# Kernel optimization log

Hardware: AMD Instinct MI355X
Metric: run time of the kernel (lower is better)

Reference implementation:

```python
import jax, jax.numpy as jnp
import numpy as np

NUM_HEADS = 8
EPS = 1e-5  # torch GroupNorm default eps


def setup_inputs() -> dict:
    key = jax.random.key(0)
    ks = jax.random.split(key, 3)
    B, C, H, W = 8, 384, 32, 32
    x = jax.random.normal(ks[0], (B, C, H, W), dtype=jnp.float32)
    qkv_w = jax.random.normal(ks[1], (3 * C, C), dtype=jnp.float32) * 0.02
    proj_w = jax.random.normal(ks[2], (C, C), dtype=jnp.float32) * 0.02
    proj_b = jnp.zeros((C,), dtype=jnp.float32)
    lambda_param = jnp.ones((1, NUM_HEADS, 1, 1), dtype=jnp.float32) * 0.5
    gc = NUM_HEADS * ((C // NUM_HEADS) // 2)  # 192 group-norm channels
    gn_weight = jnp.ones((gc,), dtype=jnp.float32)
    gn_bias = jnp.zeros((gc,), dtype=jnp.float32)
    return {"x": x, "qkv_w": qkv_w, "lambda_param": lambda_param,
            "gn_weight": gn_weight, "gn_bias": gn_bias,
            "proj_w": proj_w, "proj_b": proj_b}


def reference(x, qkv_w, lambda_param, gn_weight, gn_bias, proj_w, proj_b):
    B, C, H, W = x.shape
    nh = NUM_HEADS
    hd = C // nh
    hd2 = hd // 2
    N = H * W
    scale = hd ** -0.5

    xf = x.reshape(B, C, N)
    qkv = jnp.einsum('oc,bcn->bon', qkv_w, xf)  # (B, 3C, N), 1x1 conv no bias
    q, k, v = jnp.split(qkv, 3, axis=1)
    q = q.reshape(B, nh, hd, N)
    k = k.reshape(B, nh, hd, N)
    v = v.reshape(B, nh, hd, N)

    q1, q2 = q[:, :, :hd2], q[:, :, hd2:]
    k1, k2 = k[:, :, :hd2], k[:, :, hd2:]
    v1, v2 = v[:, :, :hd2], v[:, :, hd2:]

    # GroupNorm(2 groups) on q2 viewed as (B, nh*hd2, H, W)
    gc = nh * hd2
    qg = q2.reshape(B, 2, (gc // 2) * N)  # normalize over (group channels, H, W)
    mean = qg.mean(axis=2, keepdims=True)
    var = qg.var(axis=2, keepdims=True)
    qg = (qg - mean) * jax.lax.rsqrt(var + EPS)
    q2n = qg.reshape(B, gc, N) * gn_weight[None, :, None] + gn_bias[None, :, None]
    q2n = q2n.reshape(B, nh, hd2, N)

    # dual softmax attention maps (B, nh, N, N)
    attn1 = jax.nn.softmax(jnp.einsum('bhdn,bhdm->bhnm', q1, k1) * scale, axis=-1)
    attn2 = jax.nn.softmax(jnp.einsum('bhdn,bhdm->bhnm', q2n, k2) * scale * lambda_param, axis=-1)
    diff = attn1 - attn2

    out1 = jnp.einsum('bhnm,bhdm->bhnd', diff, v1)  # (B, nh, N, hd2)
    out2 = jnp.einsum('bhnm,bhdm->bhnd', diff, v2)
    out = jnp.concatenate([out1, out2], axis=2)  # (B, nh, 2N, hd2) -- matches torch cat dim=2
    out = out.reshape(B, C, H, W)

    out = jnp.einsum('oc,bchw->bohw', proj_w, out) + proj_b[None, :, None, None]
    return out
```

## Files before the change

### kernel.cpp

```cpp
#include <hip/hip_runtime.h>
#include <hip/hip_bf16.h>
#include <stdint.h>

typedef _Float16 half8 __attribute__((ext_vector_type(8)));
typedef _Float16 half4 __attribute__((ext_vector_type(4)));
typedef __fp16 fp16x2 __attribute__((ext_vector_type(2)));
typedef float floatx4 __attribute__((ext_vector_type(4)));
typedef float floatx16 __attribute__((ext_vector_type(16)));

#define SCALE 0.14433756729740643f
#define LOG2E 1.4426950408889634f


__device__ inline float fexp2(float x) { return __builtin_exp2f(x); }

__device__ inline uint32_t pkrtz(float a, float b) {
  fp16x2 h = __builtin_amdgcn_cvt_pkrtz(a, b);
  union { fp16x2 h; uint32_t u; } cv; cv.h = h; return cv.u;
}

__launch_bounds__(256)
__global__ void k_prep(const float* __restrict__ qkv_w, const float* __restrict__ pw,
                       const float* __restrict__ x, _Float16* __restrict__ Wf,
                       _Float16* __restrict__ PWf, _Float16* __restrict__ Xt) {
  const int bid = blockIdx.x;
  if (bid < 288) {
    const float* src = (bid < 216) ? qkv_w : pw;
    _Float16* dst = (bid < 216) ? Wf : PWf;
    int cid = (bid < 216 ? bid : bid - 216) * 256 + threadIdx.x;
    int nchunks = (bid < 216) ? 55296 : 18432;
    if (cid >= nchunks) return;
    int lane = cid & 63;
    int t = cid >> 6;
    int cb = t % 12;
    int g16 = t / 12;
    const float* s = src + (long)(g16 * 16 + (lane & 15)) * 384 + cb * 32 + (lane >> 4) * 8;
    floatx4 a = *(const floatx4*)s;
    floatx4 b = *(const floatx4*)(s + 4);
    half8 h;
    #pragma unroll
    for (int j = 0; j < 4; j++) { h[j] = (_Float16)a[j]; h[j+4] = (_Float16)b[j]; }
    *(half8*)(dst + (long)cid * 8) = h;
  } else {
    int idx = bid - 288;
    const int cblk = idx % 12, nseg = (idx / 12) & 3, b = idx / 48;
    const float* S = x + ((long)b * 384 + cblk * 32) * 1024 + nseg * 256;
    _Float16* D = Xt + (long)b * 393216 + cblk * 32768 + (long)nseg * 256 * 32;
    __shared__ _Float16 T[32][264];
    const int wv = threadIdx.x >> 6, lane = threadIdx.x & 63;
    #pragma unroll
    for (int rr = 0; rr < 8; rr++) {
      int r = wv * 8 + rr;
      floatx4 v = *(const floatx4*)(S + (long)r * 1024 + lane * 4);
      half4 h;
      #pragma unroll
      for (int j = 0; j < 4; j++) h[j] = (_Float16)v[j];
      *(half4*)&T[r][lane * 4] = h;
    }
    __syncthreads();
    const int nn = threadIdx.x >> 3, c = (threadIdx.x & 7) * 4;
    #pragma unroll
    for (int p = 0; p < 8; p++) {
      int n = p * 32 + nn;
      half4 h;
      #pragma unroll
      for (int i = 0; i < 4; i++) h[i] = T[c + i][n];
      *(half4*)(D + (long)n * 32 + c) = h;
    }
  }
}

__launch_bounds__(256)
__global__ void k_tr(const float* __restrict__ src, _Float16* __restrict__ dst) {
  const int cblk = blockIdx.x, nseg = blockIdx.y, b = blockIdx.z;
  const float* S = src + ((long)b * 384 + cblk * 32) * 1024 + nseg * 256;
  _Float16* D = dst + (long)b * 393216 + cblk * 32768 + (long)nseg * 256 * 32;
  __shared__ _Float16 T[32][264];
  const int wv = threadIdx.x >> 6, lane = threadIdx.x & 63;
  #pragma unroll
  for (int rr = 0; rr < 8; rr++) {
    int r = wv * 8 + rr;
    floatx4 v = *(const floatx4*)(S + (long)r * 1024 + lane * 4);
    half4 h;
    #pragma unroll
    for (int j = 0; j < 4; j++) h[j] = (_Float16)v[j];
    *(half4*)&T[r][lane * 4] = h;
  }
  __syncthreads();
  const int nn = threadIdx.x >> 3, c = (threadIdx.x & 7) * 4;
  #pragma unroll
  for (int p = 0; p < 8; p++) {
    int n = p * 32 + nn;
    half4 h;
    #pragma unroll
    for (int i = 0; i < 4; i++) h[i] = T[c + i][n];
    *(half4*)(D + (long)n * 32 + c) = h;
  }
}

__launch_bounds__(256, 4)
__global__ void k_qkv(const _Float16* __restrict__ Xt, const _Float16* __restrict__ Wf,
                      _Float16* __restrict__ Qs, _Float16* __restrict__ Ks,
                      _Float16* __restrict__ Vs) {
  const int tid = threadIdx.x;
  const int lane = tid & 63;
  const int wv = tid >> 6;
  const int l15 = lane & 15;
  const int g = lane >> 4;
  const int o0 = blockIdx.x * 48;
  const int n0 = blockIdx.y * 64;
  const int b = blockIdx.z;

  const int ncol = n0 + wv * 16 + l15;
  const _Float16* xp = Xt + (long)b * 393216 + (long)ncol * 32 + g * 8;
  const _Float16* wfb = Wf + (long)(blockIdx.x * 36) * 512 + lane * 8;

  half8 xb[12];
  #pragma unroll
  for (int cb = 0; cb < 12; cb++) xb[cb] = *(const half8*)(xp + cb * 32768);

  floatx4 zero4 = {0.f, 0.f, 0.f, 0.f};
  floatx4 acc0 = zero4, acc1 = zero4, acc2 = zero4;

  half8 A0 = *(const half8*)(wfb);
  half8 A1 = *(const half8*)(wfb + 12 * 512);
  half8 A2 = *(const half8*)(wfb + 24 * 512);
  #pragma unroll
  for (int cb = 0; cb < 12; cb++) {
    half8 c0 = A0, c1 = A1, c2 = A2;
    if (cb < 11) {
      A0 = *(const half8*)(wfb + (cb + 1) * 512);
      A1 = *(const half8*)(wfb + (12 + cb + 1) * 512);
      A2 = *(const half8*)(wfb + (24 + cb + 1) * 512);
    }
    acc0 = __builtin_amdgcn_mfma_f32_16x16x32_f16(c0, xb[cb], acc0, 0, 0, 0);
    acc1 = __builtin_amdgcn_mfma_f32_16x16x32_f16(c1, xb[cb], acc1, 0, 0, 0);
    acc2 = __builtin_amdgcn_mfma_f32_16x16x32_f16(c2, xb[cb], acc2, 0, 0, 0);
  }

  floatx4 acc[3] = {acc0, acc1, acc2};
  __shared__ __align__(16) _Float16 T[3456];

  if (o0 < 768) {
    #pragma unroll
    for (int rt = 0; rt < 3; rt++)
      #pragma unroll
      for (int r = 0; r < 4; r++)
        T[(wv * 16 + l15) * 52 + rt * 16 + g * 4 + r] = (_Float16)acc[rt][r];
    __syncthreads();
    const int qk = o0 >= 384;
    const int hh = (o0 - qk * 384) / 48;
    _Float16* base = (qk ? Ks : Qs) + (long)(b * 8 + hh) * 65536;
    #pragma unroll
    for (int it = 0; it < 2; it++) {
      int slot = it * 256 + tid;
      int ntl = slot >> 8;
      int t   = (slot >> 6) & 3;
      int ln  = slot & 63;
      int hi_s = ln >> 5, l31_s = ln & 31;
      int n_ = ntl * 32 + l31_s;
      int c0 = t * 16 + hi_s * 8;
      half8 val;
      #pragma unroll
      for (int j = 0; j < 8; j++) {
        int col = c0 + j;
        int d48 = col < 24 ? col : col - 8;
        bool isq = (col < 24) || (col >= 32 && col < 56);
        val[j] = isq ? T[n_ * 52 + d48] : (_Float16)0;
      }
      *(half8*)(base + ((((n0 >> 5) + ntl) * 4 + t) * 64 + ln) * 8) = val;
    }
  } else {
    #pragma unroll
    for (int rt = 0; rt < 3; rt++)
      #pragma unroll
      for (int r = 0; r < 4; r++)
        T[(rt * 16 + g * 4 + r) * 72 + wv * 16 + l15] = (_Float16)acc[rt][r];
    __syncthreads();
    const int hh = (o0 - 768) / 48;
    _Float16* base = Vs + (long)(b * 8 + hh) * 65536;
    #pragma unroll
    for (int it = 0; it < 2; it++) {
      int slot = it * 256 + tid;
      int lwin = slot >> 8;
      int ckc  = (slot >> 6) & 3;
      int kc   = ckc & 1, c = ckc >> 1;
      int ln = slot & 63;
      int hi_s = ln >> 5, l31_s = ln & 31;
      int d48 = c * 32 + l31_s;
      half8 val;
      if (d48 < 48) {
        int mb = lwin * 32 + kc * 16 + hi_s * 4;
        half4 a = *(const half4*)&T[d48 * 72 + mb];
        half4 bq = *(const half4*)&T[d48 * 72 + mb + 8];
        val[0] = a[0]; val[1] = a[1]; val[2] = a[2]; val[3] = a[3];
        val[4] = bq[0]; val[5] = bq[1]; val[6] = bq[2]; val[7] = bq[3];
      } else {
        _Float16 f = (d48 == 48) ? (_Float16)1 : (_Float16)0;
        #pragma unroll
        for (int j = 0; j < 8; j++) val[j] = f;
      }
      *(half8*)(base + ((((n0 >> 5) + lwin) * 4 + ckc) * 64 + ln) * 8) = val;
    }
  }
}

__global__ void k_gnstats(const _Float16* __restrict__ Qs, float* __restrict__ partial) {
  int bg = blockIdx.x >> 3;
  int chunk = blockIdx.x & 7;
  int b = bg >> 1, grp = bg & 1;
  float s1 = 0.f, s2 = 0.f;
  #pragma unroll
  for (int k = 0; k < 6; k++) {
    int f = chunk * 1536 + k * 256 + threadIdx.x;
    int uid = f / 96;
    int slot = f - uid * 96;
    int h = grp * 4 + (uid >> 5);
    int ntile = uid & 31;
    int t = slot < 64 ? 2 : 3;
    int ln = slot < 64 ? slot : slot - 64;
    const _Float16* p = Qs + (long)(b * 8 + h) * 65536 + ((ntile * 4 + t) * 64 + ln) * 8;
    half8 v = *(const half8*)p;
    #pragma unroll
    for (int j = 0; j < 8; j++) { float x = (float)v[j]; s1 += x; s2 += x * x; }
  }
  #pragma unroll
  for (int off = 32; off > 0; off >>= 1) {
    s1 += __shfl_down(s1, off);
    s2 += __shfl_down(s2, off);
  }
  __shared__ float red[8];
  int wv = threadIdx.x >> 6;
  if ((threadIdx.x & 63) == 0) { red[wv] = s1; red[4 + wv] = s2; }
  __syncthreads();
  if (threadIdx.x == 0) {
    float S1 = red[0] + red[1] + red[2] + red[3];
    float S2 = red[4] + red[5] + red[6] + red[7];
    partial[blockIdx.x * 2]     = S1;
    partial[blockIdx.x * 2 + 1] = S2;
  }
}

__launch_bounds__(512, 4)
__global__ void k_attn(const _Float16* __restrict__ Qs, const _Float16* __restrict__ Ks,
                       const _Float16* __restrict__ Vs, const float* __restrict__ partial,
                       const float* __restrict__ lam, const float* __restrict__ gw,
                       const float* __restrict__ gb, float* __restrict__ Y) {
  const int tid = threadIdx.x;
  const int lane = tid & 63;
  const int wv = tid >> 6;
  const int l31 = lane & 31;
  const int hi = lane >> 5;
  const int id = blockIdx.x;
  const int bh = ((id >> 6) << 3) | (id & 7);
  const int ntlgrp = (id >> 3) & 7;
  const int br = wv & 1;
  const int ntile = ntlgrp * 4 + (wv >> 1);
  const int n0 = ntile * 32;
  const int b = bh >> 3, h = bh & 7;

  const _Float16* Qp = Qs + (long)bh * 65536 + (ntile * 256 + lane) * 8;
  half8 qra = *(const half8*)(Qp + (2 * br) * 512);
  half8 qrb = *(const half8*)(Qp + (2 * br + 1) * 512);
  half8 qfa, qfb;
  if (br == 0) {
    const float s1s = SCALE * LOG2E;
    #pragma unroll
    for (int j = 0; j < 8; j++) {
      qfa[j] = (_Float16)((float)qra[j] * s1s);
      qfb[j] = (_Float16)((float)qrb[j] * s1s);
    }
  } else {
    const int grp = h >> 2;
    const float* pp = partial + (b * 2 + grp) * 16;
    float S1 = 0.f, S2 = 0.f;
    #pragma unroll
    for (int i = 0; i < 8; i++) { S1 += pp[2*i]; S2 += pp[2*i+1]; }
    float mean = S1 * (1.f / 98304.f);
    float rstd = rsqrtf(S2 * (1.f / 98304.f) - mean * mean + 1e-5f);
    float sl = SCALE * LOG2E * lam[h];
    const float* gwp = gw + h * 24;
    const float* gbp = gb + h * 24;
    #pragma unroll
    for (int j = 0; j < 8; j++) {
      qfa[j] = (_Float16)((((float)qra[j] - mean) * rstd * gwp[hi * 8 + j] + gbp[hi * 8 + j]) * sl);
      qfb[j] = (_Float16)((((float)qrb[j] - mean) * rstd * gwp[16 + j] + gbp[16 + j]) * sl);
    }
  }

  const _Float16* gK = Ks + (long)bh * 65536 + ((wv >> 2) * 2048 + (wv & 3) * 512) + lane * 8;
  const _Float16* gV = Vs + (long)bh * 65536 + ((wv >> 2) * 2048 + (wv & 3) * 512) + lane * 8;

  __shared__ __align__(16) char smem[32768];
  const int ldsK = wv * 1024 + lane * 16;
  const int ldsV = 8192 + wv * 1024 + lane * 16;

  floatx16 z16;
  #pragma unroll
  for (int i = 0; i < 16; i++) z16[i] = 0.f;
  floatx16 accA = z16, accB = z16;

  {
    uint4 a = *(const uint4*)gK;
    uint4 c = *(const uint4*)gV;
    *(uint4*)(smem + ldsK) = a;
    *(uint4*)(smem + ldsV) = c;
  }
  __syncthreads();

  #pragma unroll 2
  for (int i = 0; i < 16; i++) {
    const int cur = (i & 1) << 14;
    uint4 sa, sc;
    if (i < 15) {
      sa = *(const uint4*)(gK + (i + 1) * 4096);
      sc = *(const uint4*)(gV + (i + 1) * 4096);
    }
    #pragma unroll
    for (int j = 0; j < 2; j++) {
      const char* Kb = smem + cur + j * 4096;
      const char* Vb = smem + cur + 8192 + j * 4096;
      half8 kfa = *(const half8*)(Kb + (2 * br) * 1024 + lane * 16);
      half8 kfb = *(const half8*)(Kb + (2 * br + 1) * 1024 + lane * 16);

      floatx16 s = __builtin_amdgcn_mfma_f32_32x32x16_f16(kfa, qfa, z16, 0, 0, 0);
      s = __builtin_amdgcn_mfma_f32_32x32x16_f16(kfb, qfb, s, 0, 0, 0);

      half8 vf0 = *(const half8*)(Vb + lane * 16);
      half8 vf1 = *(const half8*)(Vb + 1024 + lane * 16);
      half8 vf2 = *(const half8*)(Vb + 2048 + lane * 16);
      half8 vf3 = *(const half8*)(Vb + 3072 + lane * 16);

      uint32_t u[8];
      #pragma unroll
      for (int q = 0; q < 8; q++)
        u[q] = pkrtz(fexp2(s[2 * q]), fexp2(s[2 * q + 1]));

      union { uint32_t u[4]; half8 h; } pa;
      pa.u[0] = u[0]; pa.u[1] = u[1]; pa.u[2] = u[2]; pa.u[3] = u[3];
      half8 pc0 = pa.h;
      pa.u[0] = u[4]; pa.u[1] = u[5]; pa.u[2] = u[6]; pa.u[3] = u[7];
      half8 pc1 = pa.h;

      accA = __builtin_amdgcn_mfma_f32_32x32x16_f16(pc0, vf0, accA, 0, 0, 0);
      accA = __builtin_amdgcn_mfma_f32_32x32x16_f16(pc1, vf1, accA, 0, 0, 0);
      accB = __builtin_amdgcn_mfma_f32_32x32x16_f16(pc0, vf2, accB, 0, 0, 0);
      accB = __builtin_amdgcn_mfma_f32_32x32x16_f16(pc1, vf3, accB, 0, 0, 0);
    }
    if (i < 15) {
      *(uint4*)(smem + (cur ^ 16384) + ldsK) = sa;
      *(uint4*)(smem + (cur ^ 16384) + ldsV) = sc;
    }
    __syncthreads();
  }

  const int pairid = wv >> 1;
  float* rbuf = (float*)(smem + pairid * 8192);
  if (br == 1) {
    #pragma unroll
    for (int r = 0; r < 16; r++) {
      rbuf[r * 64 + lane] = accA[r];
      rbuf[(16 + r) * 64 + lane] = accB[r];
    }
  }
  __syncthreads();
  if (br == 0) {
    float a2a[16], a2b[16];
    #pragma unroll
    for (int r = 0; r < 16; r++) {
      a2a[r] = rbuf[r * 64 + lane];
      a2b[r] = rbuf[(16 + r) * 64 + lane];
    }
    float* Ybh = Y + (long)bh * 49152;
    const int src = (lane & 32) + 16;
    #pragma unroll
    for (int r = 0; r < 16; r++) {
      float i1 = __builtin_amdgcn_rcpf(__shfl(accB[r], src));
      float i2 = __builtin_amdgcn_rcpf(__shfl(a2b[r], src));
      int n = n0 + (r & 3) + 8 * ((r >> 2) & 3) + 4 * hi;
      float o0 = accA[r] * i1 - a2a[r] * i2;
      float o1 = accB[r] * i1 - a2b[r] * i2;
      int p0 = l31 >= 24;
      Ybh[p0 * 24576 + n * 24 + (l31 - p0 * 24)] = o0;
      if (l31 < 16) Ybh[24576 + n * 24 + 8 + l31] = o1;
    }
  }
}

__launch_bounds__(256, 4)
__global__ void k_proj(const _Float16* __restrict__ Yt, const _Float16* __restrict__ PWf,
                       const float* __restrict__ PB, float* __restrict__ out) {
  const int tid = threadIdx.x, lane = tid & 63, wv = tid >> 6, l15 = lane & 15, g = lane >> 4;
  const int o0 = blockIdx.x * 64, m0 = blockIdx.y * 64, b = blockIdx.z;

  const int mcol = m0 + wv * 16 + l15;
  const _Float16* yp = Yt + (long)b * 393216 + (long)mcol * 32 + g * 8;
  const _Float16* wfb = PWf + (long)(blockIdx.x * 48) * 512 + lane * 8;

  half8 yb[12];
  #pragma unroll
  for (int cb = 0; cb < 12; cb++) yb[cb] = *(const half8*)(yp + cb * 32768);

  floatx4 zero4 = {0.f, 0.f, 0.f, 0.f};
  floatx4 acc0 = zero4, acc1 = zero4, acc2 = zero4, acc3 = zero4;

  half8 A0 = *(const half8*)(wfb);
  half8 A1 = *(const half8*)(wfb + 12 * 512);
  half8 A2 = *(const half8*)(wfb + 24 * 512);
  half8 A3 = *(const half8*)(wfb + 36 * 512);
  #pragma unroll
  for (int cb = 0; cb < 12; cb++) {
    half8 c0 = A0, c1 = A1, c2 = A2, c3 = A3;
    if (cb < 11) {
      A0 = *(const half8*)(wfb + (cb + 1) * 512);
      A1 = *(const half8*)(wfb + (12 + cb + 1) * 512);
      A2 = *(const half8*)(wfb + (24 + cb + 1) * 512);
      A3 = *(const half8*)(wfb + (36 + cb + 1) * 512);
    }
    acc0 = __builtin_amdgcn_mfma_f32_16x16x32_f16(c0, yb[cb], acc0, 0, 0, 0);
    acc1 = __builtin_amdgcn_mfma_f32_16x16x32_f16(c1, yb[cb], acc1, 0, 0, 0);
    acc2 = __builtin_amdgcn_mfma_f32_16x16x32_f16(c2, yb[cb], acc2, 0, 0, 0);
    acc3 = __builtin_amdgcn_mfma_f32_16x16x32_f16(c3, yb[cb], acc3, 0, 0, 0);
  }

  floatx4 acc[4] = {acc0, acc1, acc2, acc3};
  #pragma unroll
  for (int rt = 0; rt < 4; rt++) {
    int o_ = o0 + rt * 16 + g * 4;
    #pragma unroll
    for (int r = 0; r < 4; r++) {
      out[(long)(b * 384 + o_ + r) * 1024 + mcol] = acc[rt][r] + PB[o_ + r];
    }
  }
}

extern "C" void kernel_launch(void* const* d_in, const int* in_sizes, int n_in,
                              void* d_out, int out_size, void* d_ws, size_t ws_size,
                              hipStream_t stream) {
  const float* x     = (const float*)d_in[0];
  const float* qkv_w = (const float*)d_in[1];
  const float* lam   = (const float*)d_in[2];
  const float* gw    = (const float*)d_in[3];
  const float* gb    = (const float*)d_in[4];
  const float* pw    = (const float*)d_in[5];
  const float* pb    = (const float*)d_in[6];
  float* out = (float*)d_out;
  char* ws = (char*)d_ws;
  _Float16* Qs  = (_Float16*)ws;
  _Float16* Ks  = (_Float16*)(ws + 8388608);
  _Float16* Vs  = (_Float16*)(ws + 16777216);
  float* Y        = (float*)(ws + 25165824);
  float* partial  = (float*)(ws + 37748736);
  _Float16* Xt  = (_Float16*)(ws + 37752832);
  _Float16* Yt  = (_Float16*)(ws + 44044288);
  _Float16* Wf  = (_Float16*)(ws + 50335744);
  _Float16* PWf = (_Float16*)(ws + 51220480);

  hipLaunchKernelGGL(k_prep,    dim3(672),        dim3(256), 0, stream, qkv_w, pw, x, Wf, PWf, Xt);
  hipLaunchKernelGGL(k_qkv,     dim3(24, 16, 8),  dim3(256), 0, stream, Xt, Wf, Qs, Ks, Vs);
  hipLaunchKernelGGL(k_gnstats, dim3(128),        dim3(256), 0, stream, Qs, partial);
  hipLaunchKernelGGL(k_attn,    dim3(512),        dim3(512), 0, stream, Qs, Ks, Vs, partial, lam, gw, gb, Y);
  hipLaunchKernelGGL(k_tr,      dim3(12, 4, 8),   dim3(256), 0, stream, Y, Yt);
  hipLaunchKernelGGL(k_proj,    dim3(6, 16, 8),   dim3(256), 0, stream, Yt, PWf, pb, out);
}
```

Before: 96.01 us.

## Fuse GroupNorm stats into QKV kernel and transpose output into attention epilogue

Computes per-block GroupNorm partial sums inside the QKV GEMM from the shared-memory tile, removing the separate stats kernel and its re-read of Q. The attention epilogue now writes fp16 output directly in the transposed layout the projection kernel consumes, removing the fp32 intermediate and the transpose kernel. This drops two launches and a round-trip of the intermediate through global memory. The cost is scattered 2-byte stores from attention and an extra reduction and barrier in the QKV blocks.

Result: slower. 97.94 us (+2.0%).

```diff
diff --git a/kernel.cpp b/kernel.cpp
--- a/kernel.cpp
+++ b/kernel.cpp
@@ -70,38 +70,10 @@
   }
 }
 
-__launch_bounds__(256)
-__global__ void k_tr(const float* __restrict__ src, _Float16* __restrict__ dst) {
-  const int cblk = blockIdx.x, nseg = blockIdx.y, b = blockIdx.z;
-  const float* S = src + ((long)b * 384 + cblk * 32) * 1024 + nseg * 256;
-  _Float16* D = dst + (long)b * 393216 + cblk * 32768 + (long)nseg * 256 * 32;
-  __shared__ _Float16 T[32][264];
-  const int wv = threadIdx.x >> 6, lane = threadIdx.x & 63;
-  #pragma unroll
-  for (int rr = 0; rr < 8; rr++) {
-    int r = wv * 8 + rr;
-    floatx4 v = *(const floatx4*)(S + (long)r * 1024 + lane * 4);
-    half4 h;
-    #pragma unroll
-    for (int j = 0; j < 4; j++) h[j] = (_Float16)v[j];
-    *(half4*)&T[r][lane * 4] = h;
-  }
-  __syncthreads();
-  const int nn = threadIdx.x >> 3, c = (threadIdx.x & 7) * 4;
-  #pragma unroll
-  for (int p = 0; p < 8; p++) {
-    int n = p * 32 + nn;
-    half4 h;
-    #pragma unroll
-    for (int i = 0; i < 4; i++) h[i] = T[c + i][n];
-    *(half4*)(D + (long)n * 32 + c) = h;
-  }
-}
-
 __launch_bounds__(256, 4)
 __global__ void k_qkv(const _Float16* __restrict__ Xt, const _Float16* __restrict__ Wf,
                       _Float16* __restrict__ Qs, _Float16* __restrict__ Ks,
-                      _Float16* __restrict__ Vs) {
+                      _Float16* __restrict__ Vs, float* __restrict__ gnpart) {
   const int tid = threadIdx.x;
   const int lane = tid & 63;
   const int wv = tid >> 6;
@@ -140,6 +112,7 @@
 
   floatx4 acc[3] = {acc0, acc1, acc2};
   __shared__ __align__(16) _Float16 T[3456];
+  __shared__ float red[8];
 
   if (o0 < 768) {
     #pragma unroll
@@ -169,6 +142,27 @@
         val[j] = isq ? T[n_ * 52 + d48] : (_Float16)0;
       }
       *(half8*)(base + ((((n0 >> 5) + ntl) * 4 + t) * 64 + ln) * 8) = val;
+    }
+    if (!qk) {
+      float s1 = 0.f, s2 = 0.f;
+      int n_ = tid >> 2, k0 = (tid & 3) * 6;
+      #pragma unroll
+      for (int k = 0; k < 6; k++) {
+        float v = (float)T[n_ * 52 + 24 + k0 + k];
+        s1 += v; s2 += v * v;
+      }
+      #pragma unroll
+      for (int off = 32; off > 0; off >>= 1) {
+        s1 += __shfl_down(s1, off);
+        s2 += __shfl_down(s2, off);
+      }
+      if ((tid & 63) == 0) { red[tid >> 6] = s1; red[4 + (tid >> 6)] = s2; }
+      __syncthreads();
+      if (tid == 0) {
+        int slot = (b * 8 + hh) * 16 + (n0 >> 6);
+        gnpart[slot * 2]     = red[0] + red[1] + red[2] + red[3];
+        gnpart[slot * 2 + 1] = red[4] + red[5] + red[6] + red[7];
+      }
     }
   } else {
     #pragma unroll
@@ -205,47 +199,11 @@
   }
 }
 
-__global__ void k_gnstats(const _Float16* __restrict__ Qs, float* __restrict__ partial) {
-  int bg = blockIdx.x >> 3;
-  int chunk = blockIdx.x & 7;
-  int b = bg >> 1, grp = bg & 1;
-  float s1 = 0.f, s2 = 0.f;
-  #pragma unroll
-  for (int k = 0; k < 6; k++) {
-    int f = chunk * 1536 + k * 256 + threadIdx.x;
-    int uid = f / 96;
-    int slot = f - uid * 96;
-    int h = grp * 4 + (uid >> 5);
-    int ntile = uid & 31;
-    int t = slot < 64 ? 2 : 3;
-    int ln = slot < 64 ? slot : slot - 64;
-    const _Float16* p = Qs + (long)(b * 8 + h) * 65536 + ((ntile * 4 + t) * 64 + ln) * 8;
-    half8 v = *(const half8*)p;
-    #pragma unroll
-    for (int j = 0; j < 8; j++) { float x = (float)v[j]; s1 += x; s2 += x * x; }
-  }
-  #pragma unroll
-  for (int off = 32; off > 0; off >>= 1) {
-    s1 += __shfl_down(s1, off);
-    s2 += __shfl_down(s2, off);
-  }
-  __shared__ float red[8];
-  int wv = threadIdx.x >> 6;
-  if ((threadIdx.x & 63) == 0) { red[wv] = s1; red[4 + wv] = s2; }
-  __syncthreads();
-  if (threadIdx.x == 0) {
-    float S1 = red[0] + red[1] + red[2] + red[3];
-    float S2 = red[4] + red[5] + red[6] + red[7];
-    partial[blockIdx.x * 2]     = S1;
-    partial[blockIdx.x * 2 + 1] = S2;
-  }
-}
-
 __launch_bounds__(512, 4)
 __global__ void k_attn(const _Float16* __restrict__ Qs, const _Float16* __restrict__ Ks,
-                       const _Float16* __restrict__ Vs, const float* __restrict__ partial,
+                       const _Float16* __restrict__ Vs, const float* __restrict__ gnpart,
                        const float* __restrict__ lam, const float* __restrict__ gw,
-                       const float* __restrict__ gb, float* __restrict__ Y) {
+                       const float* __restrict__ gb, _Float16* __restrict__ Yt) {
   const int tid = threadIdx.x;
   const int lane = tid & 63;
   const int wv = tid >> 6;
@@ -272,10 +230,13 @@
     }
   } else {
     const int grp = h >> 2;
-    const float* pp = partial + (b * 2 + grp) * 16;
-    float S1 = 0.f, S2 = 0.f;
-    #pragma unroll
-    for (int i = 0; i < 8; i++) { S1 += pp[2*i]; S2 += pp[2*i+1]; }
+    const float* pp = gnpart + (b * 128 + grp * 64) * 2;
+    float S1 = pp[lane * 2], S2 = pp[lane * 2 + 1];
+    #pragma unroll
+    for (int off = 1; off < 64; off <<= 1) {
+      S1 += __shfl_xor(S1, off);
+      S2 += __shfl_xor(S2, off);
+    }
     float mean = S1 * (1.f / 98304.f);
     float rstd = rsqrtf(S2 * (1.f / 98304.f) - mean * mean + 1e-5f);
     float sl = SCALE * LOG2E * lam[h];
@@ -371,18 +332,25 @@
       a2a[r] = rbuf[r * 64 + lane];
       a2b[r] = rbuf[(16 + r) * 64 + lane];
     }
-    float* Ybh = Y + (long)bh * 49152;
+    _Float16* Ytb = Yt + (long)b * 393216;
+    const int hbase = h * 49152;
     const int src = (lane & 32) + 16;
     #pragma unroll
     for (int r = 0; r < 16; r++) {
       float i1 = __builtin_amdgcn_rcpf(__shfl(accB[r], src));
       float i2 = __builtin_amdgcn_rcpf(__shfl(a2b[r], src));
       int n = n0 + (r & 3) + 8 * ((r >> 2) & 3) + 4 * hi;
-      float o0 = accA[r] * i1 - a2a[r] * i2;
-      float o1 = accB[r] * i1 - a2b[r] * i2;
+      float o0v = accA[r] * i1 - a2a[r] * i2;
+      float o1v = accB[r] * i1 - a2b[r] * i2;
       int p0 = l31 >= 24;
-      Ybh[p0 * 24576 + n * 24 + (l31 - p0 * 24)] = o0;
-      if (l31 < 16) Ybh[24576 + n * 24 + 8 + l31] = o1;
+      int G0 = hbase + p0 * 24576 + n * 24 + (l31 - p0 * 24);
+      int ch0 = G0 >> 10, ny0 = G0 & 1023;
+      Ytb[(ch0 >> 5) * 32768 + ny0 * 32 + (ch0 & 31)] = (_Float16)o0v;
+      if (l31 < 16) {
+        int G1 = hbase + 24576 + n * 24 + 8 + l31;
+        int ch1 = G1 >> 10, ny1 = G1 & 1023;
+        Ytb[(ch1 >> 5) * 32768 + ny1 * 32 + (ch1 & 31)] = (_Float16)o1v;
+      }
     }
   }
 }
@@ -449,17 +417,14 @@
   _Float16* Qs  = (_Float16*)ws;
   _Float16* Ks  = (_Float16*)(ws + 8388608);
   _Float16* Vs  = (_Float16*)(ws + 16777216);
-  float* Y        = (float*)(ws + 25165824);
-  float* partial  = (float*)(ws + 37748736);
+  float* gnpart   = (float*)(ws + 25165824);
   _Float16* Xt  = (_Float16*)(ws + 37752832);
   _Float16* Yt  = (_Float16*)(ws + 44044288);
   _Float16* Wf  = (_Float16*)(ws + 50335744);
   _Float16* PWf = (_Float16*)(ws + 51220480);
 
   hipLaunchKernelGGL(k_prep,    dim3(672),        dim3(256), 0, stream, qkv_w, pw, x, Wf, PWf, Xt);
-  hipLaunchKernelGGL(k_qkv,     dim3(24, 16, 8),  dim3(256), 0, stream, Xt, Wf, Qs, Ks, Vs);
-  hipLaunchKernelGGL(k_gnstats, dim3(128),        dim3(256), 0, stream, Qs, partial);
-  hipLaunchKernelGGL(k_attn,    dim3(512),        dim3(512), 0, stream, Qs, Ks, Vs, partial, lam, gw, gb, Y);
-  hipLaunchKernelGGL(k_tr,      dim3(12, 4, 8),   dim3(256), 0, stream, Y, Yt);
+  hipLaunchKernelGGL(k_qkv,     dim3(24, 16, 8),  dim3(256), 0, stream, Xt, Wf, Qs, Ks, Vs, gnpart);
+  hipLaunchKernelGGL(k_attn,    dim3(512),        dim3(512), 0, stream, Qs, Ks, Vs, gnpart, lam, gw, gb, Yt);
   hipLaunchKernelGGL(k_proj,    dim3(6, 16, 8),   dim3(256), 0, stream, Yt, PWf, pb, out);
 }
```
